# Kernel tuning notes

Measured on AMD Instinct MI355X. Metric: run time of the kernel, lower is better.

Reference implementation:

```python
import jax, jax.numpy as jnp
import numpy as np

NEG = -9e15
SLOPE = 0.02

def setup_inputs() -> dict:
    key = jax.random.key(0)
    k1, k2, k3, k4 = jax.random.split(key, 4)
    N, IN, OUT = 16384, 128, 64
    x = jax.random.normal(k1, (N, IN), dtype=jnp.float32)
    adj = jax.random.randint(k2, (N, N), 0, 2, dtype=jnp.int32)
    weight = jax.random.normal(k3, (IN, OUT), dtype=jnp.float32) * (1.0 / np.sqrt(IN))
    att_weight = jax.random.normal(k4, (2 * OUT, 1), dtype=jnp.float32) * (1.0 / np.sqrt(2 * OUT))
    return {"x": x, "adj": adj, "weight": weight, "att_weight": att_weight}

def reference(x, adj, weight, att_weight):
    out_feature = weight.shape[1]
    Wh = x @ weight                                   # [N, out]
    f_i = Wh @ att_weight[:out_feature, :]            # [N, 1] source term
    f_j = Wh @ att_weight[out_feature:, :]            # [N, 1] dest term
    e = f_i + f_j.T                                   # [N, N] additive scores
    e = jax.nn.leaky_relu(e, negative_slope=SLOPE)
    att = jnp.where(adj > 0, e, NEG)
    att = jax.nn.softmax(att, axis=1)                 # masked row softmax
    h_prime = att @ Wh                                # [N, out]
    return jax.nn.elu(h_prime)                        # concat=True -> elu
```

## Files before the change

### kernel.cpp

```cpp
#include <hip/hip_runtime.h>
#include <cstdint>
#include <cstddef>

#define GN   16384
#define GIN  128
#define GOUT 64
#define LOG2E 1.44269504088896340736f

typedef __attribute__((ext_vector_type(8))) short short8;
typedef __attribute__((ext_vector_type(4))) float f32x4;
typedef __attribute__((ext_vector_type(4))) int   int4v;

__device__ __forceinline__ unsigned short f2bf(float f) {
  unsigned u = __float_as_uint(f);
  return (unsigned short)((u + 0x8000u) >> 16);
}

__device__ __forceinline__ unsigned short f2bf_rne(float f) {
  unsigned u = __float_as_uint(f);
  u += 0x7FFFu + ((u >> 16) & 1u);
  return (unsigned short)(u >> 16);
}

__global__ __launch_bounds__(256) void prep_kernel(
    const float* __restrict__ x, const float* __restrict__ w,
    const float* __restrict__ aw, unsigned short* __restrict__ whbt,
    float* __restrict__ fs2, float* __restrict__ fd2)
{
  __shared__ float ws[GIN * GOUT];
  __shared__ float red[2][64][4];

  const int t = threadIdx.x;
  const int rb = blockIdx.x * 64;

  for (int i = t; i < (GIN * GOUT) / 4; i += 256)
    ((float4*)ws)[i] = ((const float4*)w)[i];
  __syncthreads();

  const int r = t & 63, s = t >> 6;
  const int row = rb + r;
  const float* xr = x + (size_t)row * GIN;

  float acc[16];
#pragma unroll
  for (int d = 0; d < 16; ++d) acc[d] = 0.f;

  for (int kk = 0; kk < GIN; kk += 4) {
    float4 xv = *(const float4*)(xr + kk);
    float xa[4] = {xv.x, xv.y, xv.z, xv.w};
#pragma unroll
    for (int u = 0; u < 4; ++u) {
#pragma unroll
      for (int d = 0; d < 16; ++d)
        acc[d] += xa[u] * ws[(kk + u) * GOUT + s * 16 + d];
    }
  }

  float psrc = 0.f, pdst = 0.f;
#pragma unroll
  for (int d = 0; d < 16; ++d) {
    const int dg = s * 16 + d;
    psrc += acc[d] * aw[dg];
    pdst += acc[d] * aw[GOUT + dg];
    whbt[(size_t)dg * GN + row] = f2bf_rne(acc[d]);
  }
  red[0][r][s] = psrc;
  red[1][r][s] = pdst;
  __syncthreads();
  if (s == 0) {
    float a_ = red[0][r][0] + red[0][r][1] + red[0][r][2] + red[0][r][3];
    float b_ = red[1][r][0] + red[1][r][1] + red[1][r][2] + red[1][r][3];
    fs2[row] = a_ * LOG2E;
    fd2[row] = b_ * LOG2E;
  }
}

__global__ __launch_bounds__(256) void gat_main(
    const int* __restrict__ adj, const unsigned short* __restrict__ whbt,
    const float* __restrict__ fs2, const float* __restrict__ fd2,
    float* __restrict__ num, float* __restrict__ den)
{
  const int wave  = blockIdx.x * 4 + (threadIdx.x >> 6);
  const int lane  = threadIdx.x & 63;
  const int strip = wave & 511;
  const int chunk = wave >> 9;
  const int m = lane & 15;
  const int q = lane >> 4;
  const int row0 = strip * 32 + m;
  const int row1 = row0 + 16;

  const float fs0 = fs2[row0];
  const float fs1 = fs2[row1];
  const int CW = GN / 8;
  const int j0 = chunk * CW;

  const int4v*  __restrict__ arow0 = (const int4v*)(adj + (size_t)row0 * GN);
  const int4v*  __restrict__ arow1 = (const int4v*)(adj + (size_t)row1 * GN);
  const float4* __restrict__ fdv   = (const float4*)fd2;

  f32x4 acc0a = {0,0,0,0}, acc1a = {0,0,0,0}, acc2a = {0,0,0,0}, acc3a = {0,0,0,0};
  f32x4 acc0b = {0,0,0,0}, acc1b = {0,0,0,0}, acc2b = {0,0,0,0}, acc3b = {0,0,0,0};
  f32x4 accda = {0,0,0,0}, accdb = {0,0,0,0};

  short8 b_ones;
#pragma unroll
  for (int i = 0; i < 8; ++i) b_ones[i] = (short)0x3F80;

  auto pcalc = [&](int a, float fd, float fs) -> unsigned short {
    float sv = fs + fd;
    float lv = fmaxf(sv, 0.02f * sv);
    float pe = __builtin_amdgcn_exp2f(lv);
    pe = (a != 0) ? pe : 0.f;
    return f2bf(pe);
  };

  auto mk_af = [&](int4v aA, int4v aB, float4 fA, float4 fB, float fs) -> short8 {
    short8 af;
    af[0] = (short)pcalc(aA.x, fA.x, fs);
    af[1] = (short)pcalc(aA.y, fA.y, fs);
    af[2] = (short)pcalc(aA.z, fA.z, fs);
    af[3] = (short)pcalc(aA.w, fA.w, fs);
    af[4] = (short)pcalc(aB.x, fB.x, fs);
    af[5] = (short)pcalc(aB.y, fB.y, fs);
    af[6] = (short)pcalc(aB.z, fB.z, fs);
    af[7] = (short)pcalc(aB.w, fB.w, fs);
    return af;
  };

#pragma unroll 2
  for (int j = j0; j < j0 + CW; j += 32) {
    const int i4 = (j >> 2) + (q << 1);
    int4v a00 = __builtin_nontemporal_load(arow0 + i4);
    int4v a01 = __builtin_nontemporal_load(arow0 + i4 + 1);
    int4v a10 = __builtin_nontemporal_load(arow1 + i4);
    int4v a11 = __builtin_nontemporal_load(arow1 + i4 + 1);
    float4 f0 = fdv[i4];
    float4 f1 = fdv[i4 + 1];

    const unsigned short* wb = whbt + j + q * 8;
    short8 b0 = *(const short8*)(wb + (size_t)(0  + m) * GN);
    short8 b1 = *(const short8*)(wb + (size_t)(16 + m) * GN);
    short8 b2 = *(const short8*)(wb + (size_t)(32 + m) * GN);
    short8 b3 = *(const short8*)(wb + (size_t)(48 + m) * GN);

    short8 af0 = mk_af(a00, a01, f0, f1, fs0);
    short8 af1 = mk_af(a10, a11, f0, f1, fs1);

    acc0a = __builtin_amdgcn_mfma_f32_16x16x32_bf16(af0, b0, acc0a, 0, 0, 0);
    acc1a = __builtin_amdgcn_mfma_f32_16x16x32_bf16(af0, b1, acc1a, 0, 0, 0);
    acc2a = __builtin_amdgcn_mfma_f32_16x16x32_bf16(af0, b2, acc2a, 0, 0, 0);
    acc3a = __builtin_amdgcn_mfma_f32_16x16x32_bf16(af0, b3, acc3a, 0, 0, 0);
    accda = __builtin_amdgcn_mfma_f32_16x16x32_bf16(af0, b_ones, accda, 0, 0, 0);
    acc0b = __builtin_amdgcn_mfma_f32_16x16x32_bf16(af1, b0, acc0b, 0, 0, 0);
    acc1b = __builtin_amdgcn_mfma_f32_16x16x32_bf16(af1, b1, acc1b, 0, 0, 0);
    acc2b = __builtin_amdgcn_mfma_f32_16x16x32_bf16(af1, b2, acc2b, 0, 0, 0);
    acc3b = __builtin_amdgcn_mfma_f32_16x16x32_bf16(af1, b3, acc3b, 0, 0, 0);
    accdb = __builtin_amdgcn_mfma_f32_16x16x32_bf16(af1, b_ones, accdb, 0, 0, 0);
  }

  if (m == 0) {
#pragma unroll
    for (int r = 0; r < 4; ++r) {
      unsafeAtomicAdd(&den[strip * 32 + q * 4 + r],      accda[r]);
      unsafeAtomicAdd(&den[strip * 32 + 16 + q * 4 + r], accdb[r]);
    }
  }

  const int orow0 = strip * 32 + q * 4;
#pragma unroll
  for (int r = 0; r < 4; ++r) {
    float* nra = num + (size_t)(orow0 + r) * GOUT + m;
    unsafeAtomicAdd(nra + 0,  acc0a[r]);
    unsafeAtomicAdd(nra + 16, acc1a[r]);
    unsafeAtomicAdd(nra + 32, acc2a[r]);
    unsafeAtomicAdd(nra + 48, acc3a[r]);
    float* nrb = num + (size_t)(orow0 + 16 + r) * GOUT + m;
    unsafeAtomicAdd(nrb + 0,  acc0b[r]);
    unsafeAtomicAdd(nrb + 16, acc1b[r]);
    unsafeAtomicAdd(nrb + 32, acc2b[r]);
    unsafeAtomicAdd(nrb + 48, acc3b[r]);
  }
}

__global__ __launch_bounds__(256) void fin_kernel(
    const float* __restrict__ num, const float* __restrict__ den,
    float* __restrict__ out)
{
  const int g = blockIdx.x * 256 + threadIdx.x;
  if (g < GN * GOUT) {
    float v = num[g] / den[g >> 6];
    out[g] = (v > 0.f) ? v : expm1f(v);
  }
}

extern "C" void kernel_launch(void* const* d_in, const int* in_sizes, int n_in,
                              void* d_out, int out_size, void* d_ws, size_t ws_size,
                              hipStream_t stream) {
  const float* x   = (const float*)d_in[0];
  const int*   adj = (const int*)d_in[1];
  const float* w   = (const float*)d_in[2];
  const float* aw  = (const float*)d_in[3];
  float* out = (float*)d_out;

  float* num = (float*)d_ws;
  float* den = num + (size_t)GN * GOUT;
  float* fs2 = den + GN;
  float* fd2 = fs2 + GN;
  unsigned short* whbt = (unsigned short*)(fd2 + GN);

  hipMemsetAsync(num, 0, ((size_t)GN * GOUT + GN) * sizeof(float), stream);
  prep_kernel<<<GN / 64, 256, 0, stream>>>(x, w, aw, whbt, fs2, fd2);
  gat_main<<<(GN / 32) * 8 / 4, 256, 0, stream>>>(adj, whbt, fs2, fd2, num, den);
  fin_kernel<<<(GN * GOUT) / 256, 256, 0, stream>>>(num, den, out);
}
```

Measured before the change: 1.489 ms.

## Compress adjacency to a bitmask in a separate pass before main kernel

Adds a kernel that streams the int32 adjacency matrix once and packs it into a 1-bit-per-edge bitmask. The main attention kernel then reads 32-bit mask words instead of int4 vectors. This takes the heavy adjacency stream out of the MFMA loop, which may let that loop become compute-bound. The same 1 GB read still happens, now plus a small bitmask write and read and an extra launch, so the total may not drop if the original loop was already bandwidth-bound.

```diff
diff --git a/kernel.cpp b/kernel.cpp
--- a/kernel.cpp
+++ b/kernel.cpp
@@ -75,8 +75,25 @@
   }
 }
 
+__global__ __launch_bounds__(256) void adj_compress(
+    const int* __restrict__ adj, unsigned* __restrict__ bm)
+{
+  const size_t t = (size_t)blockIdx.x * 256 + threadIdx.x;
+  const int4v* p = (const int4v*)adj + t * 8;
+  unsigned b = 0;
+#pragma unroll
+  for (int k = 0; k < 8; ++k) {
+    int4v a = __builtin_nontemporal_load(p + k);
+    b |= (a.x != 0) ? (1u << (4 * k + 0)) : 0u;
+    b |= (a.y != 0) ? (1u << (4 * k + 1)) : 0u;
+    b |= (a.z != 0) ? (1u << (4 * k + 2)) : 0u;
+    b |= (a.w != 0) ? (1u << (4 * k + 3)) : 0u;
+  }
+  bm[t] = b;
+}
+
 __global__ __launch_bounds__(256) void gat_main(
-    const int* __restrict__ adj, const unsigned short* __restrict__ whbt,
+    const unsigned* __restrict__ bm, const unsigned short* __restrict__ whbt,
     const float* __restrict__ fs2, const float* __restrict__ fd2,
     float* __restrict__ num, float* __restrict__ den)
 {
@@ -94,9 +111,10 @@
   const int CW = GN / 8;
   const int j0 = chunk * CW;
 
-  const int4v*  __restrict__ arow0 = (const int4v*)(adj + (size_t)row0 * GN);
-  const int4v*  __restrict__ arow1 = (const int4v*)(adj + (size_t)row1 * GN);
-  const float4* __restrict__ fdv   = (const float4*)fd2;
+  const unsigned* __restrict__ bmr0 = bm + (size_t)row0 * (GN / 32);
+  const unsigned* __restrict__ bmr1 = bm + (size_t)row1 * (GN / 32);
+  const float4*   __restrict__ fdv  = (const float4*)fd2;
+  const unsigned bsh = q * 8;
 
   f32x4 acc0a = {0,0,0,0}, acc1a = {0,0,0,0}, acc2a = {0,0,0,0}, acc3a = {0,0,0,0};
   f32x4 acc0b = {0,0,0,0}, acc1b = {0,0,0,0}, acc2b = {0,0,0,0}, acc3b = {0,0,0,0};
@@ -106,34 +124,32 @@
 #pragma unroll
   for (int i = 0; i < 8; ++i) b_ones[i] = (short)0x3F80;
 
-  auto pcalc = [&](int a, float fd, float fs) -> unsigned short {
+  auto pcalc = [&](unsigned bit, float fd, float fs) -> unsigned short {
     float sv = fs + fd;
     float lv = fmaxf(sv, 0.02f * sv);
     float pe = __builtin_amdgcn_exp2f(lv);
-    pe = (a != 0) ? pe : 0.f;
+    pe = bit ? pe : 0.f;
     return f2bf(pe);
   };
 
-  auto mk_af = [&](int4v aA, int4v aB, float4 fA, float4 fB, float fs) -> short8 {
+  auto mk_af = [&](unsigned mk, float4 fA, float4 fB, float fs) -> short8 {
     short8 af;
-    af[0] = (short)pcalc(aA.x, fA.x, fs);
-    af[1] = (short)pcalc(aA.y, fA.y, fs);
-    af[2] = (short)pcalc(aA.z, fA.z, fs);
-    af[3] = (short)pcalc(aA.w, fA.w, fs);
-    af[4] = (short)pcalc(aB.x, fB.x, fs);
-    af[5] = (short)pcalc(aB.y, fB.y, fs);
-    af[6] = (short)pcalc(aB.z, fB.z, fs);
-    af[7] = (short)pcalc(aB.w, fB.w, fs);
+    af[0] = (short)pcalc(mk & 1u,   fA.x, fs);
+    af[1] = (short)pcalc(mk & 2u,   fA.y, fs);
+    af[2] = (short)pcalc(mk & 4u,   fA.z, fs);
+    af[3] = (short)pcalc(mk & 8u,   fA.w, fs);
+    af[4] = (short)pcalc(mk & 16u,  fB.x, fs);
+    af[5] = (short)pcalc(mk & 32u,  fB.y, fs);
+    af[6] = (short)pcalc(mk & 64u,  fB.z, fs);
+    af[7] = (short)pcalc(mk & 128u, fB.w, fs);
     return af;
   };
 
 #pragma unroll 2
   for (int j = j0; j < j0 + CW; j += 32) {
+    const unsigned u0 = bmr0[j >> 5] >> bsh;
+    const unsigned u1 = bmr1[j >> 5] >> bsh;
     const int i4 = (j >> 2) + (q << 1);
-    int4v a00 = __builtin_nontemporal_load(arow0 + i4);
-    int4v a01 = __builtin_nontemporal_load(arow0 + i4 + 1);
-    int4v a10 = __builtin_nontemporal_load(arow1 + i4);
-    int4v a11 = __builtin_nontemporal_load(arow1 + i4 + 1);
     float4 f0 = fdv[i4];
     float4 f1 = fdv[i4 + 1];
 
@@ -143,8 +159,8 @@
     short8 b2 = *(const short8*)(wb + (size_t)(32 + m) * GN);
     short8 b3 = *(const short8*)(wb + (size_t)(48 + m) * GN);
 
-    short8 af0 = mk_af(a00, a01, f0, f1, fs0);
-    short8 af1 = mk_af(a10, a11, f0, f1, fs1);
+    short8 af0 = mk_af(u0, f0, f1, fs0);
+    short8 af1 = mk_af(u1, f0, f1, fs1);
 
     acc0a = __builtin_amdgcn_mfma_f32_16x16x32_bf16(af0, b0, acc0a, 0, 0, 0);
     acc1a = __builtin_amdgcn_mfma_f32_16x16x32_bf16(af0, b1, acc1a, 0, 0, 0);
@@ -207,9 +223,11 @@
   float* fs2 = den + GN;
   float* fd2 = fs2 + GN;
   unsigned short* whbt = (unsigned short*)(fd2 + GN);
+  unsigned* bm = (unsigned*)(whbt + (size_t)GOUT * GN);
 
   hipMemsetAsync(num, 0, ((size_t)GN * GOUT + GN) * sizeof(float), stream);
   prep_kernel<<<GN / 64, 256, 0, stream>>>(x, w, aw, whbt, fs2, fd2);
-  gat_main<<<(GN / 32) * 8 / 4, 256, 0, stream>>>(adj, whbt, fs2, fd2, num, den);
+  adj_compress<<<(GN / 32) * (GN / 256), 256, 0, stream>>>(adj, bm);
+  gat_main<<<(GN / 32) * 8 / 4, 256, 0, stream>>>(bm, whbt, fs2, fd2, num, den);
   fin_kernel<<<(GN * GOUT) / 256, 256, 0, stream>>>(num, den, out);
 }
```

Result: slower. 1.767 ms (+18.7%).
